# Kernel tuning notes

Measured on AMD Instinct MI355X. Metric: run time of the kernel, lower is better.

The kernel has to match this reference:

```python
import jax, jax.numpy as jnp
import numpy as np

N = 20000      # nodes
E = 160000     # edges (avg degree 16)
IN_DIM = 256
HID = 128      # hidden_dim == per-head out_channels in PyG TransformerConv
HEADS = 4
EPS = 1e-5


def setup_inputs() -> dict:
    key = jax.random.key(0)
    ks = jax.random.split(key, 24)

    def w(k, shape, scale=0.05):
        return jax.random.normal(k, shape, dtype=jnp.float32) * scale

    inp = {
        "x": jax.random.normal(ks[0], (N, IN_DIM), dtype=jnp.float32),
        "edge_index": jax.random.randint(ks[1], (2, E), 0, N, dtype=jnp.int32),
        # input projection
        "lin_w": w(ks[2], (IN_DIM, HID)), "lin_b": jnp.zeros((HID,), jnp.float32),
    }
    i = 3
    for l in (1, 2):
        inp[f"q_w{l}"] = w(ks[i], (HID, HEADS * HID)); i += 1
        inp[f"q_b{l}"] = jnp.zeros((HEADS * HID,), jnp.float32)
        inp[f"k_w{l}"] = w(ks[i], (HID, HEADS * HID)); i += 1
        inp[f"k_b{l}"] = jnp.zeros((HEADS * HID,), jnp.float32)
        inp[f"v_w{l}"] = w(ks[i], (HID, HEADS * HID)); i += 1
        inp[f"v_b{l}"] = jnp.zeros((HEADS * HID,), jnp.float32)
        inp[f"s_w{l}"] = w(ks[i], (HID, HID)); i += 1
        inp[f"s_b{l}"] = jnp.zeros((HID,), jnp.float32)
        inp[f"ln_g{l}"] = jnp.ones((HID,), jnp.float32)
        inp[f"ln_b{l}"] = jnp.zeros((HID,), jnp.float32)
    return inp


def _segment_softmax(scores, seg, num):
    # scores: [E, HEADS], seg: [E] destination indices
    m = jax.ops.segment_max(scores, seg, num_segments=num)
    m = jnp.where(jnp.isfinite(m), m, 0.0)  # guard empty segments
    e = jnp.exp(scores - m[seg])
    d = jax.ops.segment_sum(e, seg, num_segments=num)
    return e / (d[seg] + 1e-16)


def _transformer_conv(x, src, dst, qw, qb, kw, kb, vw, vb, sw, sb):
    # PyG TransformerConv(HID, HID, heads=HEADS, concat=False)
    n = x.shape[0]
    q = (x @ qw + qb).reshape(n, HEADS, HID)
    k = (x @ kw + kb).reshape(n, HEADS, HID)
    v = (x @ vw + vb).reshape(n, HEADS, HID)
    # per-edge attention: query at dst (i), key/value at src (j)
    alpha = jnp.einsum("ehd,ehd->eh", q[dst], k[src]) / jnp.sqrt(jnp.float32(HID))
    alpha = _segment_softmax(alpha, dst, n)                 # [E, HEADS]
    msg = v[src] * alpha[..., None]                          # [E, HEADS, HID]
    out = jax.ops.segment_sum(msg, dst, num_segments=n)      # [N, HEADS, HID]
    out = out.mean(axis=1)                                   # concat=False -> head mean
    return out + x @ sw + sb                                 # root skip connection


def _layer_norm(x, g, b):
    mu = x.mean(-1, keepdims=True)
    var = ((x - mu) ** 2).mean(-1, keepdims=True)
    return (x - mu) * jax.lax.rsqrt(var + EPS) * g + b


def reference(x, edge_index, lin_w, lin_b,
              q_w1, q_b1, k_w1, k_b1, v_w1, v_b1, s_w1, s_b1, ln_g1, ln_b1,
              q_w2, q_b2, k_w2, k_b2, v_w2, v_b2, s_w2, s_b2, ln_g2, ln_b2):
    src, dst = edge_index[0], edge_index[1]
    h = jax.nn.relu(x @ lin_w + lin_b)
    h1 = _transformer_conv(h, src, dst, q_w1, q_b1, k_w1, k_b1, v_w1, v_b1, s_w1, s_b1)
    h = _layer_norm(h1 + h, ln_g1, ln_b1)
    h2 = _transformer_conv(h, src, dst, q_w2, q_b2, k_w2, k_b2, v_w2, v_b2, s_w2, s_b2)
    h = _layer_norm(h2 + h, ln_g2, ln_b2)
    return h
```

## Files before the change

### kernel.cpp

```cpp
#include <hip/hip_runtime.h>
#include <math.h>

#define NNODE 20000
#define NEDGE 160000
#define IN_DIMV 256
#define HIDV 128
#define DEGCAP 64
#define BAT 4

typedef __attribute__((ext_vector_type(8))) short bf16x8;
typedef __attribute__((ext_vector_type(4))) float f32x4;
typedef __attribute__((ext_vector_type(2))) float f32x2;

__device__ __forceinline__ float bf2f(unsigned short u) {
    union { unsigned int i; float f; } x; x.i = ((unsigned int)u) << 16; return x.f;
}
__device__ __forceinline__ unsigned short f2bf(float f) {
    union { float f; unsigned int i; } x; x.f = f;
    unsigned int r = x.i + 0x7fffu + ((x.i >> 16) & 1u);
    return (unsigned short)(r >> 16);
}
__device__ __forceinline__ void unpack8(uint4 p, float* f) {
    f[0] = bf2f((unsigned short)(p.x & 0xffff)); f[1] = bf2f((unsigned short)(p.x >> 16));
    f[2] = bf2f((unsigned short)(p.y & 0xffff)); f[3] = bf2f((unsigned short)(p.y >> 16));
    f[4] = bf2f((unsigned short)(p.z & 0xffff)); f[5] = bf2f((unsigned short)(p.z >> 16));
    f[6] = bf2f((unsigned short)(p.w & 0xffff)); f[7] = bf2f((unsigned short)(p.w >> 16));
}
__device__ __forceinline__ void unpack8f8_w(unsigned int a, unsigned int b, float* f) {
    f32x2 t;
    t = __builtin_amdgcn_cvt_pk_f32_fp8((int)a, false); f[0] = t.x; f[1] = t.y;
    t = __builtin_amdgcn_cvt_pk_f32_fp8((int)a, true);  f[2] = t.x; f[3] = t.y;
    t = __builtin_amdgcn_cvt_pk_f32_fp8((int)b, false); f[4] = t.x; f[5] = t.y;
    t = __builtin_amdgcn_cvt_pk_f32_fp8((int)b, true);  f[6] = t.x; f[7] = t.y;
}
__device__ __forceinline__ unsigned char f2fp8(float v) {
    int pk = __builtin_amdgcn_cvt_pk_fp8_f32(v, v, 0, false);
    return (unsigned char)(pk & 0xff);
}
__device__ __forceinline__ void gld_lds16(const unsigned short* g, unsigned short* l) {
    __builtin_amdgcn_global_load_lds((const __attribute__((address_space(1))) void*)g,
                                     (__attribute__((address_space(3))) void*)l, 16, 0, 0);
}

__global__ void convert_kernel(
    const float* __restrict__ lin_w,
    const float* __restrict__ qw0, const float* __restrict__ kw0,
    const float* __restrict__ vw0, const float* __restrict__ sw0,
    const float* __restrict__ qw1, const float* __restrict__ kw1,
    const float* __restrict__ vw1, const float* __restrict__ sw1,
    unsigned short* __restrict__ arena, int* __restrict__ cursor)
{
    int idx = blockIdx.x * 256 + threadIdx.x;
    if (idx < NNODE) cursor[idx] = 0;
    int id2 = idx - NNODE;
    if (id2 < 0 || id2 >= 458752) return;
    float v;
    if (id2 < 32768) {
        int n = id2 >> 8, k = id2 & 255;
        v = lin_w[k * 128 + n];
    } else {
        int t = id2 - 32768;
        int l = t / 212992, r = t % 212992;
        int n = r >> 7, k = r & 127;
        const float* qw = l ? qw1 : qw0;
        const float* kw = l ? kw1 : kw0;
        const float* vw = l ? vw1 : vw0;
        const float* sw = l ? sw1 : sw0;
        if (n < 1536) {
            const float* w = (n < 512) ? qw : (n < 1024) ? kw : vw;
            v = w[k * 512 + (n & 511)];
        } else {
            v = sw[k * 128 + (n - 1536)];
        }
    }
    arena[id2] = f2bf(v);
}

__global__ __launch_bounds__(256) void mfma_gemm0(
    const float* __restrict__ A, const unsigned short* __restrict__ WT,
    const float* __restrict__ b0, unsigned short* __restrict__ hbf_out)
{
    __shared__ unsigned short smem[8192];
    unsigned short* As = smem;
    unsigned short* Bs = smem + 4096;
    unsigned short* ot = smem;
    const int K = 256;

    int tid = threadIdx.x;
    int lane = tid & 63;
    int w = tid >> 6;
    int wm = w & 1, wn = w >> 1;
    int bm = blockIdx.x * 128;

    int r0 = tid >> 2;
    int c0 = (tid & 3) * 8;
    int g0 = bm + r0;      if (g0 > NNODE - 1) g0 = NNODE - 1;
    int g1 = bm + r0 + 64; if (g1 > NNODE - 1) g1 = NNODE - 1;
    int srow = lane >> 2;
    int scol = (lane & 3) * 8;
    int br0 = w * 32 + srow;
    int br1 = w * 32 + 16 + srow;

    f32x4 acc[4][4] = {};
    int arow = wm * 64 + (lane & 15);
    int brow = wn * 64 + (lane & 15);
    int koff = (lane >> 4) * 8;

    for (int k0 = 0; k0 < K; k0 += 32) {
        {
            const float4* p0 = (const float4*)(A + (size_t)g0 * K + k0 + c0);
            float4 u = p0[0], v = p0[1];
            unsigned short t0[8] = {f2bf(u.x), f2bf(u.y), f2bf(u.z), f2bf(u.w),
                                    f2bf(v.x), f2bf(v.y), f2bf(v.z), f2bf(v.w)};
            *(uint4*)&As[r0 * 32 + c0] = *(uint4*)t0;
            const float4* p1 = (const float4*)(A + (size_t)g1 * K + k0 + c0);
            u = p1[0]; v = p1[1];
            unsigned short t1[8] = {f2bf(u.x), f2bf(u.y), f2bf(u.z), f2bf(u.w),
                                    f2bf(v.x), f2bf(v.y), f2bf(v.z), f2bf(v.w)};
            *(uint4*)&As[(r0 + 64) * 32 + c0] = *(uint4*)t1;
        }
        gld_lds16(WT + (size_t)br0 * K + k0 + scol, Bs + (w * 32) * 32);
        gld_lds16(WT + (size_t)br1 * K + k0 + scol, Bs + (w * 32 + 16) * 32);
        __syncthreads();
        bf16x8 fa[4], fb[4];
#pragma unroll
        for (int i = 0; i < 4; i++) fa[i] = *(const bf16x8*)&As[(arow + i * 16) * 32 + koff];
#pragma unroll
        for (int i = 0; i < 4; i++) fb[i] = *(const bf16x8*)&Bs[(brow + i * 16) * 32 + koff];
#pragma unroll
        for (int mi = 0; mi < 4; mi++)
#pragma unroll
            for (int ni = 0; ni < 4; ni++)
                acc[mi][ni] = __builtin_amdgcn_mfma_f32_16x16x32_bf16(fa[mi], fb[ni], acc[mi][ni], 0, 0, 0);
        __syncthreads();
    }

    int quad = lane >> 4, lcol = lane & 15;
#pragma unroll
    for (int hh = 0; hh < 2; hh++) {
        __syncthreads();
        if (wm == hh) {
#pragma unroll
            for (int mi = 0; mi < 4; mi++) {
#pragma unroll
                for (int ni = 0; ni < 4; ni++) {
                    int lc = wn * 64 + ni * 16 + lcol;
                    float bias = b0[lc];
#pragma unroll
                    for (int reg = 0; reg < 4; reg++) {
                        float v = fmaxf(acc[mi][ni][reg] + bias, 0.f);
                        ot[(mi * 16 + quad * 4 + reg) * 128 + lc] = f2bf(v);
                    }
                }
            }
        }
        __syncthreads();
        int r = tid >> 2, ch = tid & 3;
        int row = bm + hh * 64 + r;
        if (row < NNODE) {
            uint4* dp = (uint4*)(hbf_out + (size_t)row * HIDV + ch * 32);
            const uint4* sp = (const uint4*)(ot + r * 128 + ch * 32);
#pragma unroll
            for (int q = 0; q < 4; q++) dp[q] = sp[q];
        }
    }
}

__global__ __launch_bounds__(256) void mfma_gemm1(
    const unsigned short* __restrict__ A, const unsigned short* __restrict__ WT,
    const float* __restrict__ b0, const float* __restrict__ b1,
    const float* __restrict__ b2, const float* __restrict__ b3,
    unsigned short* __restrict__ qb_out, unsigned char* __restrict__ kv8_out,
    unsigned short* __restrict__ pre16_out)
{
    __shared__ unsigned short As[16384];
    __shared__ unsigned short Ws[16384];
    unsigned short* ot = Ws;
    unsigned char* ot8 = (unsigned char*)Ws;
    const int K = 128;

    int tid = threadIdx.x;
    int lane = tid & 63;
    int w = tid >> 6;
    int wm = w & 1, wn = w >> 1;
    int bm = blockIdx.x * 128;
    int p0 = (blockIdx.y == 0) ? 0 : 7;
    int p1 = (blockIdx.y == 0) ? 7 : 13;

    int srow = lane >> 2;
    int scol = (lane & 3) * 8;
    int sr0 = w * 32 + srow;
    int sr1 = w * 32 + 16 + srow;
    int ar0 = bm + sr0; if (ar0 > NNODE - 1) ar0 = NNODE - 1;
    int ar1 = bm + sr1; if (ar1 > NNODE - 1) ar1 = NNODE - 1;

#pragma unroll
    for (int c = 0; c < 4; c++) {
        int k0 = c * 32;
        gld_lds16(A + (size_t)ar0 * K + k0 + scol, As + c * 4096 + sr0 * 32);
        gld_lds16(A + (size_t)ar1 * K + k0 + scol, As + c * 4096 + sr1 * 32);
    }

    int arow = wm * 64 + (lane & 15);
    int brow = wn * 64 + (lane & 15);
    int koff = (lane >> 4) * 8;
    int quad = lane >> 4, lcol = lane & 15;

    for (int p = p0; p < p1; p++) {
        int bn = p * 128;
#pragma unroll
        for (int c = 0; c < 4; c++) {
            int k0 = c * 32;
            gld_lds16(WT + (size_t)(bn + sr0) * K + k0 + scol, Ws + c * 4096 + sr0 * 32);
            gld_lds16(WT + (size_t)(bn + sr1) * K + k0 + scol, Ws + c * 4096 + sr1 * 32);
        }
        __syncthreads();

        f32x4 acc[4][4] = {};
#pragma unroll
        for (int c = 0; c < 4; c++) {
            bf16x8 fa[4], fb[4];
#pragma unroll
            for (int i = 0; i < 4; i++) fa[i] = *(const bf16x8*)&As[c * 4096 + (arow + i * 16) * 32 + koff];
#pragma unroll
            for (int i = 0; i < 4; i++) fb[i] = *(const bf16x8*)&Ws[c * 4096 + (brow + i * 16) * 32 + koff];
#pragma unroll
            for (int mi = 0; mi < 4; mi++)
#pragma unroll
                for (int ni = 0; ni < 4; ni++)
                    acc[mi][ni] = __builtin_amdgcn_mfma_f32_16x16x32_bf16(fa[mi], fb[ni], acc[mi][ni], 0, 0, 0);
        }
        __syncthreads();

        if (p < 4 || p == 12) {
            const float* bb = (p < 4) ? (b0 + bn) : b3;
#pragma unroll
            for (int mi = 0; mi < 4; mi++) {
#pragma unroll
                for (int ni = 0; ni < 4; ni++) {
                    int lc = wn * 64 + ni * 16 + lcol;
                    float bias = bb[lc];
#pragma unroll
                    for (int reg = 0; reg < 4; reg++)
                        ot[(wm * 64 + mi * 16 + quad * 4 + reg) * 128 + lc] = f2bf(acc[mi][ni][reg] + bias);
                }
            }
            __syncthreads();
            int r = tid >> 1, hf = tid & 1;
            int row = bm + r;
            if (row < NNODE) {
                unsigned short* dst = (p < 4) ? (qb_out + (size_t)row * 512 + bn + hf * 64)
                                              : (pre16_out + (size_t)row * HIDV + hf * 64);
                const uint4* sp = (const uint4*)(ot + r * 128 + hf * 64);
                uint4* dp = (uint4*)dst;
#pragma unroll
                for (int q = 0; q < 8; q++) dp[q] = sp[q];
            }
            __syncthreads();
        } else {
            const float* bb = (bn < 1024) ? (b1 + bn - 512) : (b2 + bn - 1024);
            int coff = bn - 512;
#pragma unroll
            for (int mi = 0; mi < 4; mi++) {
#pragma unroll
                for (int ni = 0; ni < 4; ni++) {
                    int lc = wn * 64 + ni * 16 + lcol;
                    float bias = bb[lc];
#pragma unroll
                    for (int reg = 0; reg < 4; reg++)
                        ot8[(wm * 64 + mi * 16 + quad * 4 + reg) * 128 + lc] = f2fp8(acc[mi][ni][reg] + bias);
                }
            }
            __syncthreads();
            int r = tid >> 1, hf = tid & 1;
            int row = bm + r;
            if (row < NNODE) {
                uint4* dp = (uint4*)(kv8_out + (size_t)row * 1024 + coff + hf * 64);
                const uint4* sp = (const uint4*)(ot8 + r * 128 + hf * 64);
#pragma unroll
                for (int q = 0; q < 4; q++) dp[q] = sp[q];
            }
            __syncthreads();
        }
    }
}

__global__ void scatter_kernel(const int* __restrict__ ei, int* __restrict__ cursor,
                               int* __restrict__ bucket) {
    int e = blockIdx.x * blockDim.x + threadIdx.x;
    if (e < NEDGE) {
        int d = ei[NEDGE + e];
        int slot = atomicAdd(&cursor[d], 1);
        if (slot < DEGCAP) bucket[d * DEGCAP + slot] = ei[e];
    }
}

__global__ __launch_bounds__(256) void attn_ln_kernel(
    const unsigned short* __restrict__ qb, const unsigned char* __restrict__ kv8,
    const int* __restrict__ cursor, const int* __restrict__ bucket,
    const unsigned short* __restrict__ pre16, const float* __restrict__ g,
    const float* __restrict__ b,
    unsigned short* __restrict__ hbf ,
    float* __restrict__ extout)
{
    int lane = threadIdx.x & 63;
    int wid = threadIdx.x >> 6;
    int i = blockIdx.x * 4 + wid;
    int cnt = cursor[i]; if (cnt > DEGCAP) cnt = DEGCAP;
    const int* bk = bucket + i * DEGCAP;

    int hg = lane >> 4;
    int sl = lane & 15;
    int off = hg * 128 + sl * 8;

    size_t base = (size_t)i * HIDV + sl * 8;
    uint4 pv_raw = *(const uint4*)(pre16 + base);
    uint4 hv_raw = *(const uint4*)(hbf + base);

    float qr[8];
    {
        uint4 p = *(const uint4*)(qb + (size_t)i * 512 + lane * 8);
        unpack8(p, qr);
#pragma unroll
        for (int j = 0; j < 8; j++) qr[j] *= 0.0883883476483184f;
    }

    float m = -INFINITY, l = 0.f;
    float acc[8] = {0.f, 0.f, 0.f, 0.f, 0.f, 0.f, 0.f, 0.f};

    if (cnt > 0) {
        int myidx = bk[(lane < cnt) ? lane : 0];

        uint2 kA[BAT], vA[BAT], kB[BAT], vB[BAT];

        auto issue = [&](uint2 (&KB)[BAT], uint2 (&VB)[BAT], int bb) {
#pragma unroll
            for (int t = 0; t < BAT; t++) {
                int j = bb * BAT + t; if (j >= cnt) j = cnt - 1;
                int src = __shfl(myidx, j);
                const unsigned char* bp = kv8 + (size_t)src * 1024 + off;
                KB[t] = *(const uint2*)bp;
                VB[t] = *(const uint2*)(bp + 512);
            }
        };

        auto consume = [&](const uint2 (&KB)[BAT], const uint2 (&VB)[BAT], int bb) {
            int rem = cnt - bb * BAT;
            float d[BAT];
#pragma unroll
            for (int t = 0; t < BAT; t++) d[t] = -3.0e38f;
#pragma unroll
            for (int t = 0; t < BAT; t++) {
                if (t >= rem) break;
                float kf[8];
                unpack8f8_w(KB[t].x, KB[t].y, kf);
                d[t] = qr[0] * kf[0] + qr[1] * kf[1] + qr[2] * kf[2] + qr[3] * kf[3] +
                       qr[4] * kf[4] + qr[5] * kf[5] + qr[6] * kf[6] + qr[7] * kf[7];
            }
#pragma unroll
            for (int t = 0; t < BAT; t++) { if (t >= rem) break; d[t] += __shfl_xor(d[t], 8); }
#pragma unroll
            for (int t = 0; t < BAT; t++) { if (t >= rem) break; d[t] += __shfl_xor(d[t], 4); }
#pragma unroll
            for (int t = 0; t < BAT; t++) { if (t >= rem) break; d[t] += __shfl_xor(d[t], 2); }
#pragma unroll
            for (int t = 0; t < BAT; t++) { if (t >= rem) break; d[t] += __shfl_xor(d[t], 1); }

            float mq = d[0];
#pragma unroll
            for (int t = 1; t < BAT; t++) mq = fmaxf(mq, d[t]);
            float mn = fmaxf(m, mq);
            float scale = __expf(m - mn);
            float p[BAT];
            float psum = 0.f;
#pragma unroll
            for (int t = 0; t < BAT; t++) { p[t] = __expf(d[t] - mn); psum += p[t]; }
            l = l * scale + psum;
            m = mn;
#pragma unroll
            for (int c = 0; c < 8; c++) acc[c] *= scale;
#pragma unroll
            for (int t = 0; t < BAT; t++) {
                if (t >= rem) break;
                float vf[8];
                unpack8f8_w(VB[t].x, VB[t].y, vf);
                float pt = p[t];
#pragma unroll
                for (int c = 0; c < 8; c++) acc[c] += pt * vf[c];
            }
        };

        int nb = (cnt + BAT - 1) >> 2;
        issue(kA, vA, 0);
        for (int bb = 0; bb < nb; bb += 2) {
            if (bb + 1 < nb) issue(kB, vB, bb + 1);
            consume(kA, vA, bb);
            if (bb + 1 < nb) {
                if (bb + 2 < nb) issue(kA, vA, bb + 2);
                consume(kB, vB, bb + 1);
            }
        }
    }

    float linv = 0.25f / (l + 1e-16f);
#pragma unroll
    for (int c = 0; c < 8; c++) acc[c] *= linv;
#pragma unroll
    for (int c = 0; c < 8; c++) {
        acc[c] += __shfl_xor(acc[c], 16);
        acc[c] += __shfl_xor(acc[c], 32);
    }

    float pv[8], hv[8];
    unpack8(pv_raw, pv);
    unpack8(hv_raw, hv);
    float vals[8];
#pragma unroll
    for (int c = 0; c < 8; c++) vals[c] = acc[c] + pv[c] + hv[c];

    float s = 0.f;
#pragma unroll
    for (int c = 0; c < 8; c++) s += vals[c];
    s += __shfl_xor(s, 1); s += __shfl_xor(s, 2);
    s += __shfl_xor(s, 4); s += __shfl_xor(s, 8);
    float mu = s * (1.f / 128.f);
    float vs = 0.f;
#pragma unroll
    for (int c = 0; c < 8; c++) { float dx = vals[c] - mu; vs += dx * dx; }
    vs += __shfl_xor(vs, 1); vs += __shfl_xor(vs, 2);
    vs += __shfl_xor(vs, 4); vs += __shfl_xor(vs, 8);
    float rstd = rsqrtf(vs * (1.f / 128.f) + 1e-5f);

    float4 g0 = ((const float4*)(g + sl * 8))[0];
    float4 g1 = ((const float4*)(g + sl * 8))[1];
    float4 bb0 = ((const float4*)(b + sl * 8))[0];
    float4 bb1 = ((const float4*)(b + sl * 8))[1];
    float y[8];
    y[0] = (vals[0] - mu) * rstd * g0.x + bb0.x; y[1] = (vals[1] - mu) * rstd * g0.y + bb0.y;
    y[2] = (vals[2] - mu) * rstd * g0.z + bb0.z; y[3] = (vals[3] - mu) * rstd * g0.w + bb0.w;
    y[4] = (vals[4] - mu) * rstd * g1.x + bb1.x; y[5] = (vals[5] - mu) * rstd * g1.y + bb1.y;
    y[6] = (vals[6] - mu) * rstd * g1.z + bb1.z; y[7] = (vals[7] - mu) * rstd * g1.w + bb1.w;

    if (lane < 16) {
        unsigned short tmp[8] = {f2bf(y[0]), f2bf(y[1]), f2bf(y[2]), f2bf(y[3]),
                                 f2bf(y[4]), f2bf(y[5]), f2bf(y[6]), f2bf(y[7])};
        *(uint4*)(hbf + base) = *(uint4*)tmp;
        if (extout) {
            ((float4*)(extout + base))[0] = make_float4(y[0], y[1], y[2], y[3]);
            ((float4*)(extout + base))[1] = make_float4(y[4], y[5], y[6], y[7]);
        }
    }
}

extern "C" void kernel_launch(void* const* d_in, const int* in_sizes, int n_in,
                              void* d_out, int out_size, void* d_ws, size_t ws_size,
                              hipStream_t stream) {
    const float* x = (const float*)d_in[0];
    const int* ei = (const int*)d_in[1];

    char* ws = (char*)d_ws;
    unsigned short* hbf = (unsigned short*)(ws + 0);
    unsigned short* pre16 = (unsigned short*)(ws + 5120000);
    unsigned short* qb = (unsigned short*)(ws + 10240000);
    unsigned char* kv8 = (unsigned char*)(ws + 30720000);
    int* cursor = (int*)(ws + 51200000);
    int* bucket = (int*)(ws + 51280000);
    unsigned short* arena = (unsigned short*)(ws + 56400000);

    convert_kernel<<<(NNODE + 458752 + 255) / 256, 256, 0, stream>>>(
        (const float*)d_in[2],
        (const float*)d_in[4], (const float*)d_in[6], (const float*)d_in[8], (const float*)d_in[10],
        (const float*)d_in[14], (const float*)d_in[16], (const float*)d_in[18], (const float*)d_in[20],
        arena, cursor);

    scatter_kernel<<<(NEDGE + 255) / 256, 256, 0, stream>>>(ei, cursor, bucket);

    const int GM = (NNODE + 127) / 128;

    mfma_gemm0<<<GM, 256, 0, stream>>>(x, arena, (const float*)d_in[3], hbf);

    for (int l = 0; l < 2; l++) {
        int o = 4 + l * 10;
        const unsigned short* WT = arena + 32768 + l * 212992;
        mfma_gemm1<<<dim3(GM, 2), 256, 0, stream>>>(
            hbf, WT,
            (const float*)d_in[o + 1], (const float*)d_in[o + 3],
            (const float*)d_in[o + 5], (const float*)d_in[o + 7],
            qb, kv8, pre16);

        attn_ln_kernel<<<NNODE / 4, 256, 0, stream>>>(
            qb, kv8, cursor, bucket, pre16,
            (const float*)d_in[o + 8], (const float*)d_in[o + 9],
            hbf, (l == 1) ? (float*)d_out : nullptr);
    }
}
```

Before: 279.5 us.

## Interleave K/V fp8 per lane and launch one GEMM block per output tile

The fp8 K and V projections are now stored interleaved, so each lane's 8 K bytes and 8 V bytes for a head sit next to each other in a 16-byte chunk. The attention kernel then fetches both with a single 16-byte gather per edge instead of two 8-byte gathers. Separately, the QKV/skip GEMM now launches 13 column tiles in the grid instead of each block looping over 6-7 tiles. That gives more parallelism, but every block reloads its A tile. The fp8 stores from the GEMM become strided 8-byte writes.

```diff
diff --git a/kernel.cpp b/kernel.cpp
--- a/kernel.cpp
+++ b/kernel.cpp
@@ -184,8 +184,8 @@
     int w = tid >> 6;
     int wm = w & 1, wn = w >> 1;
     int bm = blockIdx.x * 128;
-    int p0 = (blockIdx.y == 0) ? 0 : 7;
-    int p1 = (blockIdx.y == 0) ? 7 : 13;
+    int p = blockIdx.y;
+    int bn = p * 128;
 
     int srow = lane >> 2;
     int scol = (lane & 3) * 8;
@@ -199,88 +199,80 @@
         int k0 = c * 32;
         gld_lds16(A + (size_t)ar0 * K + k0 + scol, As + c * 4096 + sr0 * 32);
         gld_lds16(A + (size_t)ar1 * K + k0 + scol, As + c * 4096 + sr1 * 32);
-    }
+        gld_lds16(WT + (size_t)(bn + sr0) * K + k0 + scol, Ws + c * 4096 + sr0 * 32);
+        gld_lds16(WT + (size_t)(bn + sr1) * K + k0 + scol, Ws + c * 4096 + sr1 * 32);
+    }
+    __syncthreads();
 
     int arow = wm * 64 + (lane & 15);
     int brow = wn * 64 + (lane & 15);
     int koff = (lane >> 4) * 8;
     int quad = lane >> 4, lcol = lane & 15;
 
-    for (int p = p0; p < p1; p++) {
-        int bn = p * 128;
-#pragma unroll
-        for (int c = 0; c < 4; c++) {
-            int k0 = c * 32;
-            gld_lds16(WT + (size_t)(bn + sr0) * K + k0 + scol, Ws + c * 4096 + sr0 * 32);
-            gld_lds16(WT + (size_t)(bn + sr1) * K + k0 + scol, Ws + c * 4096 + sr1 * 32);
-        }
-        __syncthreads();
-
-        f32x4 acc[4][4] = {};
-#pragma unroll
-        for (int c = 0; c < 4; c++) {
-            bf16x8 fa[4], fb[4];
-#pragma unroll
-            for (int i = 0; i < 4; i++) fa[i] = *(const bf16x8*)&As[c * 4096 + (arow + i * 16) * 32 + koff];
-#pragma unroll
-            for (int i = 0; i < 4; i++) fb[i] = *(const bf16x8*)&Ws[c * 4096 + (brow + i * 16) * 32 + koff];
-#pragma unroll
-            for (int mi = 0; mi < 4; mi++)
-#pragma unroll
-                for (int ni = 0; ni < 4; ni++)
-                    acc[mi][ni] = __builtin_amdgcn_mfma_f32_16x16x32_bf16(fa[mi], fb[ni], acc[mi][ni], 0, 0, 0);
-        }
-        __syncthreads();
-
-        if (p < 4 || p == 12) {
-            const float* bb = (p < 4) ? (b0 + bn) : b3;
-#pragma unroll
-            for (int mi = 0; mi < 4; mi++) {
-#pragma unroll
-                for (int ni = 0; ni < 4; ni++) {
-                    int lc = wn * 64 + ni * 16 + lcol;
-                    float bias = bb[lc];
-#pragma unroll
-                    for (int reg = 0; reg < 4; reg++)
-                        ot[(wm * 64 + mi * 16 + quad * 4 + reg) * 128 + lc] = f2bf(acc[mi][ni][reg] + bias);
-                }
-            }
-            __syncthreads();
-            int r = tid >> 1, hf = tid & 1;
-            int row = bm + r;
-            if (row < NNODE) {
-                unsigned short* dst = (p < 4) ? (qb_out + (size_t)row * 512 + bn + hf * 64)
-                                              : (pre16_out + (size_t)row * HIDV + hf * 64);
-                const uint4* sp = (const uint4*)(ot + r * 128 + hf * 64);
-                uint4* dp = (uint4*)dst;
-#pragma unroll
-                for (int q = 0; q < 8; q++) dp[q] = sp[q];
-            }
-            __syncthreads();
-        } else {
-            const float* bb = (bn < 1024) ? (b1 + bn - 512) : (b2 + bn - 1024);
-            int coff = bn - 512;
-#pragma unroll
-            for (int mi = 0; mi < 4; mi++) {
-#pragma unroll
-                for (int ni = 0; ni < 4; ni++) {
-                    int lc = wn * 64 + ni * 16 + lcol;
-                    float bias = bb[lc];
-#pragma unroll
-                    for (int reg = 0; reg < 4; reg++)
-                        ot8[(wm * 64 + mi * 16 + quad * 4 + reg) * 128 + lc] = f2fp8(acc[mi][ni][reg] + bias);
-                }
-            }
-            __syncthreads();
-            int r = tid >> 1, hf = tid & 1;
-            int row = bm + r;
-            if (row < NNODE) {
-                uint4* dp = (uint4*)(kv8_out + (size_t)row * 1024 + coff + hf * 64);
-                const uint4* sp = (const uint4*)(ot8 + r * 128 + hf * 64);
-#pragma unroll
-                for (int q = 0; q < 4; q++) dp[q] = sp[q];
-            }
-            __syncthreads();
+    f32x4 acc[4][4] = {};
+#pragma unroll
+    for (int c = 0; c < 4; c++) {
+        bf16x8 fa[4], fb[4];
+#pragma unroll
+        for (int i = 0; i < 4; i++) fa[i] = *(const bf16x8*)&As[c * 4096 + (arow + i * 16) * 32 + koff];
+#pragma unroll
+        for (int i = 0; i < 4; i++) fb[i] = *(const bf16x8*)&Ws[c * 4096 + (brow + i * 16) * 32 + koff];
+#pragma unroll
+        for (int mi = 0; mi < 4; mi++)
+#pragma unroll
+            for (int ni = 0; ni < 4; ni++)
+                acc[mi][ni] = __builtin_amdgcn_mfma_f32_16x16x32_bf16(fa[mi], fb[ni], acc[mi][ni], 0, 0, 0);
+    }
+    __syncthreads();
+
+    if (p < 4 || p == 12) {
+        const float* bb = (p < 4) ? (b0 + bn) : b3;
+#pragma unroll
+        for (int mi = 0; mi < 4; mi++) {
+#pragma unroll
+            for (int ni = 0; ni < 4; ni++) {
+                int lc = wn * 64 + ni * 16 + lcol;
+                float bias = bb[lc];
+#pragma unroll
+                for (int reg = 0; reg < 4; reg++)
+                    ot[(wm * 64 + mi * 16 + quad * 4 + reg) * 128 + lc] = f2bf(acc[mi][ni][reg] + bias);
+            }
+        }
+        __syncthreads();
+        int r = tid >> 1, hf = tid & 1;
+        int row = bm + r;
+        if (row < NNODE) {
+            unsigned short* dst = (p < 4) ? (qb_out + (size_t)row * 512 + bn + hf * 64)
+                                          : (pre16_out + (size_t)row * HIDV + hf * 64);
+            const uint4* sp = (const uint4*)(ot + r * 128 + hf * 64);
+            uint4* dp = (uint4*)dst;
+#pragma unroll
+            for (int q = 0; q < 8; q++) dp[q] = sp[q];
+        }
+    } else {
+        const float* bb = (bn < 1024) ? (b1 + bn - 512) : (b2 + bn - 1024);
+        int h = (p - 4) & 3;
+        int isV = (p >= 8) ? 8 : 0;
+#pragma unroll
+        for (int mi = 0; mi < 4; mi++) {
+#pragma unroll
+            for (int ni = 0; ni < 4; ni++) {
+                int lc = wn * 64 + ni * 16 + lcol;
+                float bias = bb[lc];
+#pragma unroll
+                for (int reg = 0; reg < 4; reg++)
+                    ot8[(wm * 64 + mi * 16 + quad * 4 + reg) * 128 + lc] = f2fp8(acc[mi][ni][reg] + bias);
+            }
+        }
+        __syncthreads();
+        int r = tid >> 1, hf = tid & 1;
+        int row = bm + r;
+        if (row < NNODE) {
+            const uint2* sp = (const uint2*)(ot8 + r * 128 + hf * 64);
+            unsigned char* dbase = kv8_out + (size_t)row * 1024 + h * 256 + hf * 128 + isV;
+#pragma unroll
+            for (int q = 0; q < 8; q++)
+                *(uint2*)(dbase + q * 16) = sp[q];
         }
     }
 }
@@ -311,7 +303,7 @@
 
     int hg = lane >> 4;
     int sl = lane & 15;
-    int off = hg * 128 + sl * 8;
+    int off = hg * 256 + sl * 16;
 
     size_t base = (size_t)i * HIDV + sl * 8;
     uint4 pv_raw = *(const uint4*)(pre16 + base);
@@ -331,20 +323,18 @@
     if (cnt > 0) {
         int myidx = bk[(lane < cnt) ? lane : 0];
 
-        uint2 kA[BAT], vA[BAT], kB[BAT], vB[BAT];
-
-        auto issue = [&](uint2 (&KB)[BAT], uint2 (&VB)[BAT], int bb) {
+        uint4 kvA[BAT], kvB[BAT];
+
+        auto issue = [&](uint4 (&KV)[BAT], int bb) {
 #pragma unroll
             for (int t = 0; t < BAT; t++) {
                 int j = bb * BAT + t; if (j >= cnt) j = cnt - 1;
                 int src = __shfl(myidx, j);
-                const unsigned char* bp = kv8 + (size_t)src * 1024 + off;
-                KB[t] = *(const uint2*)bp;
-                VB[t] = *(const uint2*)(bp + 512);
+                KV[t] = *(const uint4*)(kv8 + (size_t)src * 1024 + off);
             }
         };
 
-        auto consume = [&](const uint2 (&KB)[BAT], const uint2 (&VB)[BAT], int bb) {
+        auto consume = [&](const uint4 (&KV)[BAT], int bb) {
             int rem = cnt - bb * BAT;
             float d[BAT];
 #pragma unroll
@@ -353,7 +343,7 @@
             for (int t = 0; t < BAT; t++) {
                 if (t >= rem) break;
                 float kf[8];
-                unpack8f8_w(KB[t].x, KB[t].y, kf);
+                unpack8f8_w(KV[t].x, KV[t].y, kf);
                 d[t] = qr[0] * kf[0] + qr[1] * kf[1] + qr[2] * kf[2] + qr[3] * kf[3] +
                        qr[4] * kf[4] + qr[5] * kf[5] + qr[6] * kf[6] + qr[7] * kf[7];
             }
@@ -383,7 +373,7 @@
             for (int t = 0; t < BAT; t++) {
                 if (t >= rem) break;
                 float vf[8];
-                unpack8f8_w(VB[t].x, VB[t].y, vf);
+                unpack8f8_w(KV[t].z, KV[t].w, vf);
                 float pt = p[t];
 #pragma unroll
                 for (int c = 0; c < 8; c++) acc[c] += pt * vf[c];
@@ -391,13 +381,13 @@
         };
 
         int nb = (cnt + BAT - 1) >> 2;
-        issue(kA, vA, 0);
+        issue(kvA, 0);
         for (int bb = 0; bb < nb; bb += 2) {
-            if (bb + 1 < nb) issue(kB, vB, bb + 1);
-            consume(kA, vA, bb);
+            if (bb + 1 < nb) issue(kvB, bb + 1);
+            consume(kvA, bb);
             if (bb + 1 < nb) {
-                if (bb + 2 < nb) issue(kA, vA, bb + 2);
-                consume(kB, vB, bb + 1);
+                if (bb + 2 < nb) issue(kvA, bb + 2);
+                consume(kvB, bb + 1);
             }
         }
     }
@@ -482,7 +472,7 @@
     for (int l = 0; l < 2; l++) {
         int o = 4 + l * 10;
         const unsigned short* WT = arena + 32768 + l * 212992;
-        mfma_gemm1<<<dim3(GM, 2), 256, 0, stream>>>(
+        mfma_gemm1<<<dim3(GM, 13), 256, 0, stream>>>(
             hbf, WT,
             (const float*)d_in[o + 1], (const float*)d_in[o + 3],
             (const float*)d_in[o + 5], (const float*)d_in[o + 7],
```

Measured after the change: 284.6 us. About the same (+1.8%).

## Process two destination nodes per wavefront in attention kernel to overlap gathers

Applied to the files above, without the earlier changes.

Each wavefront in the attention+LayerNorm kernel now handles two destination nodes and interleaves their first two K/V gather batches, so more memory loads are in flight per wave. The aim is to hide gather latency for typical degree-16 nodes, with half as many blocks launched. The cost is higher register pressure and possibly lower occupancy. Bucket indices are now read unconditionally for all 64 lanes, even past each node's edge count.

```diff
diff --git a/kernel.cpp b/kernel.cpp
--- a/kernel.cpp
+++ b/kernel.cpp
@@ -305,151 +305,190 @@
 {
     int lane = threadIdx.x & 63;
     int wid = threadIdx.x >> 6;
-    int i = blockIdx.x * 4 + wid;
-    int cnt = cursor[i]; if (cnt > DEGCAP) cnt = DEGCAP;
-    const int* bk = bucket + i * DEGCAP;
+    int iA = blockIdx.x * 8 + wid * 2;
+    int iB = iA + 1;
+
+    int idxA = bucket[iA * DEGCAP + lane];
+    int idxB = bucket[iB * DEGCAP + lane];
+    int cntA = cursor[iA]; if (cntA > DEGCAP) cntA = DEGCAP;
+    int cntB = cursor[iB]; if (cntB > DEGCAP) cntB = DEGCAP;
 
     int hg = lane >> 4;
     int sl = lane & 15;
     int off = hg * 128 + sl * 8;
 
-    size_t base = (size_t)i * HIDV + sl * 8;
-    uint4 pv_raw = *(const uint4*)(pre16 + base);
-    uint4 hv_raw = *(const uint4*)(hbf + base);
-
-    float qr[8];
+    size_t baseA = (size_t)iA * HIDV + sl * 8;
+    size_t baseB = (size_t)iB * HIDV + sl * 8;
+    uint4 pvA_raw = *(const uint4*)(pre16 + baseA);
+    uint4 hvA_raw = *(const uint4*)(hbf + baseA);
+    uint4 pvB_raw = *(const uint4*)(pre16 + baseB);
+    uint4 hvB_raw = *(const uint4*)(hbf + baseB);
+
+    float qrA[8], qrB[8];
     {
-        uint4 p = *(const uint4*)(qb + (size_t)i * 512 + lane * 8);
-        unpack8(p, qr);
-#pragma unroll
-        for (int j = 0; j < 8; j++) qr[j] *= 0.0883883476483184f;
-    }
-
-    float m = -INFINITY, l = 0.f;
-    float acc[8] = {0.f, 0.f, 0.f, 0.f, 0.f, 0.f, 0.f, 0.f};
-
-    if (cnt > 0) {
-        int myidx = bk[(lane < cnt) ? lane : 0];
-
-        uint2 kA[BAT], vA[BAT], kB[BAT], vB[BAT];
-
-        auto issue = [&](uint2 (&KB)[BAT], uint2 (&VB)[BAT], int bb) {
-#pragma unroll
-            for (int t = 0; t < BAT; t++) {
-                int j = bb * BAT + t; if (j >= cnt) j = cnt - 1;
-                int src = __shfl(myidx, j);
-                const unsigned char* bp = kv8 + (size_t)src * 1024 + off;
-                KB[t] = *(const uint2*)bp;
-                VB[t] = *(const uint2*)(bp + 512);
-            }
-        };
-
-        auto consume = [&](const uint2 (&KB)[BAT], const uint2 (&VB)[BAT], int bb) {
-            int rem = cnt - bb * BAT;
-            float d[BAT];
-#pragma unroll
-            for (int t = 0; t < BAT; t++) d[t] = -3.0e38f;
-#pragma unroll
-            for (int t = 0; t < BAT; t++) {
-                if (t >= rem) break;
-                float kf[8];
-                unpack8f8_w(KB[t].x, KB[t].y, kf);
-                d[t] = qr[0] * kf[0] + qr[1] * kf[1] + qr[2] * kf[2] + qr[3] * kf[3] +
-                       qr[4] * kf[4] + qr[5] * kf[5] + qr[6] * kf[6] + qr[7] * kf[7];
-            }
-#pragma unroll
-            for (int t = 0; t < BAT; t++) { if (t >= rem) break; d[t] += __shfl_xor(d[t], 8); }
-#pragma unroll
-            for (int t = 0; t < BAT; t++) { if (t >= rem) break; d[t] += __shfl_xor(d[t], 4); }
-#pragma unroll
-            for (int t = 0; t < BAT; t++) { if (t >= rem) break; d[t] += __shfl_xor(d[t], 2); }
-#pragma unroll
-            for (int t = 0; t < BAT; t++) { if (t >= rem) break; d[t] += __shfl_xor(d[t], 1); }
-
-            float mq = d[0];
-#pragma unroll
-            for (int t = 1; t < BAT; t++) mq = fmaxf(mq, d[t]);
-            float mn = fmaxf(m, mq);
-            float scale = __expf(m - mn);
-            float p[BAT];
-            float psum = 0.f;
-#pragma unroll
-            for (int t = 0; t < BAT; t++) { p[t] = __expf(d[t] - mn); psum += p[t]; }
-            l = l * scale + psum;
-            m = mn;
-#pragma unroll
-            for (int c = 0; c < 8; c++) acc[c] *= scale;
-#pragma unroll
-            for (int t = 0; t < BAT; t++) {
-                if (t >= rem) break;
-                float vf[8];
-                unpack8f8_w(VB[t].x, VB[t].y, vf);
-                float pt = p[t];
-#pragma unroll
-                for (int c = 0; c < 8; c++) acc[c] += pt * vf[c];
-            }
-        };
-
-        int nb = (cnt + BAT - 1) >> 2;
-        issue(kA, vA, 0);
-        for (int bb = 0; bb < nb; bb += 2) {
-            if (bb + 1 < nb) issue(kB, vB, bb + 1);
-            consume(kA, vA, bb);
-            if (bb + 1 < nb) {
-                if (bb + 2 < nb) issue(kA, vA, bb + 2);
-                consume(kB, vB, bb + 1);
-            }
-        }
-    }
-
-    float linv = 0.25f / (l + 1e-16f);
-#pragma unroll
-    for (int c = 0; c < 8; c++) acc[c] *= linv;
-#pragma unroll
-    for (int c = 0; c < 8; c++) {
-        acc[c] += __shfl_xor(acc[c], 16);
-        acc[c] += __shfl_xor(acc[c], 32);
-    }
-
-    float pv[8], hv[8];
-    unpack8(pv_raw, pv);
-    unpack8(hv_raw, hv);
-    float vals[8];
-#pragma unroll
-    for (int c = 0; c < 8; c++) vals[c] = acc[c] + pv[c] + hv[c];
-
-    float s = 0.f;
-#pragma unroll
-    for (int c = 0; c < 8; c++) s += vals[c];
-    s += __shfl_xor(s, 1); s += __shfl_xor(s, 2);
-    s += __shfl_xor(s, 4); s += __shfl_xor(s, 8);
-    float mu = s * (1.f / 128.f);
-    float vs = 0.f;
-#pragma unroll
-    for (int c = 0; c < 8; c++) { float dx = vals[c] - mu; vs += dx * dx; }
-    vs += __shfl_xor(vs, 1); vs += __shfl_xor(vs, 2);
-    vs += __shfl_xor(vs, 4); vs += __shfl_xor(vs, 8);
-    float rstd = rsqrtf(vs * (1.f / 128.f) + 1e-5f);
-
-    float4 g0 = ((const float4*)(g + sl * 8))[0];
-    float4 g1 = ((const float4*)(g + sl * 8))[1];
-    float4 bb0 = ((const float4*)(b + sl * 8))[0];
-    float4 bb1 = ((const float4*)(b + sl * 8))[1];
-    float y[8];
-    y[0] = (vals[0] - mu) * rstd * g0.x + bb0.x; y[1] = (vals[1] - mu) * rstd * g0.y + bb0.y;
-    y[2] = (vals[2] - mu) * rstd * g0.z + bb0.z; y[3] = (vals[3] - mu) * rstd * g0.w + bb0.w;
-    y[4] = (vals[4] - mu) * rstd * g1.x + bb1.x; y[5] = (vals[5] - mu) * rstd * g1.y + bb1.y;
-    y[6] = (vals[6] - mu) * rstd * g1.z + bb1.z; y[7] = (vals[7] - mu) * rstd * g1.w + bb1.w;
-
-    if (lane < 16) {
-        unsigned short tmp[8] = {f2bf(y[0]), f2bf(y[1]), f2bf(y[2]), f2bf(y[3]),
-                                 f2bf(y[4]), f2bf(y[5]), f2bf(y[6]), f2bf(y[7])};
-        *(uint4*)(hbf + base) = *(uint4*)tmp;
-        if (extout) {
-            ((float4*)(extout + base))[0] = make_float4(y[0], y[1], y[2], y[3]);
-            ((float4*)(extout + base))[1] = make_float4(y[4], y[5], y[6], y[7]);
-        }
-    }
+        uint4 pa = *(const uint4*)(qb + (size_t)iA * 512 + lane * 8);
+        uint4 pb = *(const uint4*)(qb + (size_t)iB * 512 + lane * 8);
+        unpack8(pa, qrA);
+        unpack8(pb, qrB);
+#pragma unroll
+        for (int j = 0; j < 8; j++) { qrA[j] *= 0.0883883476483184f; qrB[j] *= 0.0883883476483184f; }
+    }
+
+    float mA = -INFINITY, lA = 0.f, mB = -INFINITY, lB = 0.f;
+    float accA[8] = {0.f, 0.f, 0.f, 0.f, 0.f, 0.f, 0.f, 0.f};
+    float accB[8] = {0.f, 0.f, 0.f, 0.f, 0.f, 0.f, 0.f, 0.f};
+
+    auto issue = [&](uint2 (&K)[BAT], uint2 (&V)[BAT], int idx, int cc, int bb) {
+#pragma unroll
+        for (int t = 0; t < BAT; t++) {
+            int j = bb * BAT + t; if (j >= cc) j = cc - 1;
+            int src = __shfl(idx, j);
+            const unsigned char* bp = kv8 + (size_t)src * 1024 + off;
+            K[t] = *(const uint2*)bp;
+            V[t] = *(const uint2*)(bp + 512);
+        }
+    };
+
+    auto consume = [&](const uint2 (&K)[BAT], const uint2 (&V)[BAT], int cc, int bb,
+                       float& m, float& l, float (&acc)[8], const float (&qr)[8]) {
+        int rem = cc - bb * BAT;
+        float d[BAT];
+#pragma unroll
+        for (int t = 0; t < BAT; t++) d[t] = -3.0e38f;
+#pragma unroll
+        for (int t = 0; t < BAT; t++) {
+            if (t >= rem) break;
+            float kf[8];
+            unpack8f8_w(K[t].x, K[t].y, kf);
+            d[t] = qr[0] * kf[0] + qr[1] * kf[1] + qr[2] * kf[2] + qr[3] * kf[3] +
+                   qr[4] * kf[4] + qr[5] * kf[5] + qr[6] * kf[6] + qr[7] * kf[7];
+        }
+#pragma unroll
+        for (int t = 0; t < BAT; t++) { if (t >= rem) break; d[t] += __shfl_xor(d[t], 8); }
+#pragma unroll
+        for (int t = 0; t < BAT; t++) { if (t >= rem) break; d[t] += __shfl_xor(d[t], 4); }
+#pragma unroll
+        for (int t = 0; t < BAT; t++) { if (t >= rem) break; d[t] += __shfl_xor(d[t], 2); }
+#pragma unroll
+        for (int t = 0; t < BAT; t++) { if (t >= rem) break; d[t] += __shfl_xor(d[t], 1); }
+
+        float mq = d[0];
+#pragma unroll
+        for (int t = 1; t < BAT; t++) mq = fmaxf(mq, d[t]);
+        float mn = fmaxf(m, mq);
+        float scale = __expf(m - mn);
+        float p[BAT];
+        float psum = 0.f;
+#pragma unroll
+        for (int t = 0; t < BAT; t++) { p[t] = __expf(d[t] - mn); psum += p[t]; }
+        l = l * scale + psum;
+        m = mn;
+#pragma unroll
+        for (int c = 0; c < 8; c++) acc[c] *= scale;
+#pragma unroll
+        for (int t = 0; t < BAT; t++) {
+            if (t >= rem) break;
+            float vf[8];
+            unpack8f8_w(V[t].x, V[t].y, vf);
+            float pt = p[t];
+#pragma unroll
+            for (int c = 0; c < 8; c++) acc[c] += pt * vf[c];
+        }
+    };
+
+    {
+        uint2 KA0[BAT], VA0[BAT], KA1[BAT], VA1[BAT];
+        uint2 KB0[BAT], VB0[BAT], KB1[BAT], VB1[BAT];
+        int nbA = (cntA + BAT - 1) >> 2;
+        int nbB = (cntB + BAT - 1) >> 2;
+
+        if (nbA > 0) issue(KA0, VA0, idxA, cntA, 0);
+        if (nbB > 0) issue(KB0, VB0, idxB, cntB, 0);
+        if (nbA > 1) issue(KA1, VA1, idxA, cntA, 1);
+        if (nbB > 1) issue(KB1, VB1, idxB, cntB, 1);
+
+        if (nbA > 0) consume(KA0, VA0, cntA, 0, mA, lA, accA, qrA);
+        if (nbB > 0) consume(KB0, VB0, cntB, 0, mB, lB, accB, qrB);
+        if (nbA > 1) consume(KA1, VA1, cntA, 1, mA, lA, accA, qrA);
+        if (nbB > 1) consume(KB1, VB1, cntB, 1, mB, lB, accB, qrB);
+
+        if (nbA > 2) {
+            issue(KA0, VA0, idxA, cntA, 2);
+            for (int bb = 2; bb < nbA; bb += 2) {
+                if (bb + 1 < nbA) issue(KA1, VA1, idxA, cntA, bb + 1);
+                consume(KA0, VA0, cntA, bb, mA, lA, accA, qrA);
+                if (bb + 1 < nbA) {
+                    if (bb + 2 < nbA) issue(KA0, VA0, idxA, cntA, bb + 2);
+                    consume(KA1, VA1, cntA, bb + 1, mA, lA, accA, qrA);
+                }
+            }
+        }
+        if (nbB > 2) {
+            issue(KB0, VB0, idxB, cntB, 2);
+            for (int bb = 2; bb < nbB; bb += 2) {
+                if (bb + 1 < nbB) issue(KB1, VB1, idxB, cntB, bb + 1);
+                consume(KB0, VB0, cntB, bb, mB, lB, accB, qrB);
+                if (bb + 1 < nbB) {
+                    if (bb + 2 < nbB) issue(KB0, VB0, idxB, cntB, bb + 2);
+                    consume(KB1, VB1, cntB, bb + 1, mB, lB, accB, qrB);
+                }
+            }
+        }
+    }
+
+    auto epilogue = [&](float lv, float (&acc)[8], uint4 pv_raw, uint4 hv_raw, size_t base) {
+        float linv = 0.25f / (lv + 1e-16f);
+#pragma unroll
+        for (int c = 0; c < 8; c++) acc[c] *= linv;
+#pragma unroll
+        for (int c = 0; c < 8; c++) {
+            acc[c] += __shfl_xor(acc[c], 16);
+            acc[c] += __shfl_xor(acc[c], 32);
+        }
+
+        float pv[8], hv[8];
+        unpack8(pv_raw, pv);
+        unpack8(hv_raw, hv);
+        float vals[8];
+#pragma unroll
+        for (int c = 0; c < 8; c++) vals[c] = acc[c] + pv[c] + hv[c];
+
+        float s = 0.f;
+#pragma unroll
+        for (int c = 0; c < 8; c++) s += vals[c];
+        s += __shfl_xor(s, 1); s += __shfl_xor(s, 2);
+        s += __shfl_xor(s, 4); s += __shfl_xor(s, 8);
+        float mu = s * (1.f / 128.f);
+        float vs = 0.f;
+#pragma unroll
+        for (int c = 0; c < 8; c++) { float dx = vals[c] - mu; vs += dx * dx; }
+        vs += __shfl_xor(vs, 1); vs += __shfl_xor(vs, 2);
+        vs += __shfl_xor(vs, 4); vs += __shfl_xor(vs, 8);
+        float rstd = rsqrtf(vs * (1.f / 128.f) + 1e-5f);
+
+        float4 g0 = ((const float4*)(g + sl * 8))[0];
+        float4 g1 = ((const float4*)(g + sl * 8))[1];
+        float4 bb0 = ((const float4*)(b + sl * 8))[0];
+        float4 bb1 = ((const float4*)(b + sl * 8))[1];
+        float y[8];
+        y[0] = (vals[0] - mu) * rstd * g0.x + bb0.x; y[1] = (vals[1] - mu) * rstd * g0.y + bb0.y;
+        y[2] = (vals[2] - mu) * rstd * g0.z + bb0.z; y[3] = (vals[3] - mu) * rstd * g0.w + bb0.w;
+        y[4] = (vals[4] - mu) * rstd * g1.x + bb1.x; y[5] = (vals[5] - mu) * rstd * g1.y + bb1.y;
+        y[6] = (vals[6] - mu) * rstd * g1.z + bb1.z; y[7] = (vals[7] - mu) * rstd * g1.w + bb1.w;
+
+        if (lane < 16) {
+            unsigned short tmp[8] = {f2bf(y[0]), f2bf(y[1]), f2bf(y[2]), f2bf(y[3]),
+                                     f2bf(y[4]), f2bf(y[5]), f2bf(y[6]), f2bf(y[7])};
+            *(uint4*)(hbf + base) = *(uint4*)tmp;
+            if (extout) {
+                ((float4*)(extout + base))[0] = make_float4(y[0], y[1], y[2], y[3]);
+                ((float4*)(extout + base))[1] = make_float4(y[4], y[5], y[6], y[7]);
+            }
+        }
+    };
+
+    epilogue(lA, accA, pvA_raw, hvA_raw, baseA);
+    epilogue(lB, accB, pvB_raw, hvB_raw, baseB);
 }
 
 extern "C" void kernel_launch(void* const* d_in, const int* in_sizes, int n_in,
@@ -488,7 +527,7 @@
             (const float*)d_in[o + 5], (const float*)d_in[o + 7],
             qb, kv8, pre16);
 
-        attn_ln_kernel<<<NNODE / 4, 256, 0, stream>>>(
+        attn_ln_kernel<<<NNODE / 8, 256, 0, stream>>>(
             qb, kv8, cursor, bucket, pre16,
             (const float*)d_in[o + 8], (const float*)d_in[o + 9],
             hbf, (l == 1) ? (float*)d_out : nullptr);
```

Result: slower. 287.8 us (+3.0%).

## Keep GEMM operand fragments in registers and prefetch next weight tile directly

Applied to the files above, without the earlier changes.

The QKV projection GEMM no longer stages weight tiles through LDS. Each wave loads its B fragments straight from global memory into registers and prefetches the next 128-column panel while the current one's MFMAs run. The A tile is read from LDS into registers once and reused across all panels, which removes the Ws buffer and the per-panel syncs. This raises register pressure (32 bf16x8 fragments held live) and uses uncoalesced per-lane global loads. Separately, the attention kernel hoists the bucket index load ahead of the count check, reading the full 64-slot row unconditionally so the load starts earlier.

```diff
diff --git a/kernel.cpp b/kernel.cpp
--- a/kernel.cpp
+++ b/kernel.cpp
@@ -174,9 +174,8 @@
     unsigned short* __restrict__ pre16_out)
 {
     __shared__ unsigned short As[16384];
-    __shared__ unsigned short Ws[16384];
-    unsigned short* ot = Ws;
-    unsigned char* ot8 = (unsigned char*)Ws;
+    unsigned short* ot = As;
+    unsigned char* ot8 = (unsigned char*)As;
     const int K = 128;
 
     int tid = threadIdx.x;
@@ -194,43 +193,56 @@
     int ar0 = bm + sr0; if (ar0 > NNODE - 1) ar0 = NNODE - 1;
     int ar1 = bm + sr1; if (ar1 > NNODE - 1) ar1 = NNODE - 1;
 
-#pragma unroll
-    for (int c = 0; c < 4; c++) {
-        int k0 = c * 32;
-        gld_lds16(A + (size_t)ar0 * K + k0 + scol, As + c * 4096 + sr0 * 32);
-        gld_lds16(A + (size_t)ar1 * K + k0 + scol, As + c * 4096 + sr1 * 32);
-    }
-
     int arow = wm * 64 + (lane & 15);
     int brow = wn * 64 + (lane & 15);
     int koff = (lane >> 4) * 8;
     int quad = lane >> 4, lcol = lane & 15;
 
+#pragma unroll
+    for (int c = 0; c < 4; c++) {
+        gld_lds16(A + (size_t)ar0 * K + c * 32 + scol, As + c * 4096 + sr0 * 32);
+        gld_lds16(A + (size_t)ar1 * K + c * 32 + scol, As + c * 4096 + sr1 * 32);
+    }
+
+    const unsigned short* Wb = WT + (size_t)brow * K + koff;
+
+    bf16x8 fb[4][4];
+#pragma unroll
+    for (int c = 0; c < 4; c++)
+#pragma unroll
+        for (int i = 0; i < 4; i++)
+            fb[c][i] = *(const bf16x8*)(Wb + (size_t)(p0 * 128 + i * 16) * K + c * 32);
+
+    __syncthreads();
+
+    bf16x8 fa[4][4];
+#pragma unroll
+    for (int c = 0; c < 4; c++)
+#pragma unroll
+        for (int i = 0; i < 4; i++)
+            fa[c][i] = *(const bf16x8*)&As[c * 4096 + (arow + i * 16) * 32 + koff];
+
+    __syncthreads();
+
     for (int p = p0; p < p1; p++) {
         int bn = p * 128;
-#pragma unroll
-        for (int c = 0; c < 4; c++) {
-            int k0 = c * 32;
-            gld_lds16(WT + (size_t)(bn + sr0) * K + k0 + scol, Ws + c * 4096 + sr0 * 32);
-            gld_lds16(WT + (size_t)(bn + sr1) * K + k0 + scol, Ws + c * 4096 + sr1 * 32);
-        }
-        __syncthreads();
 
         f32x4 acc[4][4] = {};
 #pragma unroll
-        for (int c = 0; c < 4; c++) {
-            bf16x8 fa[4], fb[4];
-#pragma unroll
-            for (int i = 0; i < 4; i++) fa[i] = *(const bf16x8*)&As[c * 4096 + (arow + i * 16) * 32 + koff];
-#pragma unroll
-            for (int i = 0; i < 4; i++) fb[i] = *(const bf16x8*)&Ws[c * 4096 + (brow + i * 16) * 32 + koff];
+        for (int c = 0; c < 4; c++)
 #pragma unroll
             for (int mi = 0; mi < 4; mi++)
 #pragma unroll
                 for (int ni = 0; ni < 4; ni++)
-                    acc[mi][ni] = __builtin_amdgcn_mfma_f32_16x16x32_bf16(fa[mi], fb[ni], acc[mi][ni], 0, 0, 0);
-        }
-        __syncthreads();
+                    acc[mi][ni] = __builtin_amdgcn_mfma_f32_16x16x32_bf16(fa[c][mi], fb[c][ni], acc[mi][ni], 0, 0, 0);
+
+        if (p + 1 < p1) {
+#pragma unroll
+            for (int c = 0; c < 4; c++)
+#pragma unroll
+                for (int i = 0; i < 4; i++)
+                    fb[c][i] = *(const bf16x8*)(Wb + (size_t)((p + 1) * 128 + i * 16) * K + c * 32);
+        }
 
         if (p < 4 || p == 12) {
             const float* bb = (p < 4) ? (b0 + bn) : b3;
@@ -306,8 +318,8 @@
     int lane = threadIdx.x & 63;
     int wid = threadIdx.x >> 6;
     int i = blockIdx.x * 4 + wid;
+    int myidx = bucket[i * DEGCAP + lane];
     int cnt = cursor[i]; if (cnt > DEGCAP) cnt = DEGCAP;
-    const int* bk = bucket + i * DEGCAP;
 
     int hg = lane >> 4;
     int sl = lane & 15;
@@ -329,8 +341,6 @@
     float acc[8] = {0.f, 0.f, 0.f, 0.f, 0.f, 0.f, 0.f, 0.f};
 
     if (cnt > 0) {
-        int myidx = bk[(lane < cnt) ? lane : 0];
-
         uint2 kA[BAT], vA[BAT], kB[BAT], vB[BAT];
 
         auto issue = [&](uint2 (&KB)[BAT], uint2 (&VB)[BAT], int bb) {
```

Result: slower. 326.1 us (+16.6%).
